# Performance work log

Measured on AMD Instinct MI355X. Metric: run time of the kernel, lower is better.

## Reference

```python
import jax, jax.numpy as jnp
import numpy as np

N = 200000   # nodes
E = 3200000  # edges
B = 1024     # graphs in batch
A = 10       # num_actions
IN, C, ED = 9, 64, 1
NEG_SLOPE = 0.2


def _xavier(k, shape):
    lim = (6.0 / (shape[0] + shape[1])) ** 0.5
    return jax.random.uniform(k, shape, jnp.float32, -lim, lim)


def setup_inputs() -> dict:
    key = jax.random.key(0)
    ks = jax.random.split(key, 24)
    x = jax.random.normal(ks[0], (N, IN), jnp.float32)
    edge_index = jax.random.randint(ks[1], (2, E), 0, N, dtype=jnp.int64)
    edge_attr = jax.random.normal(ks[2], (E, ED), jnp.float32)
    agent_state = jax.random.normal(ks[3], (B, 34), jnp.float32)
    pool_batch = jnp.sort(jax.random.randint(ks[4], (N,), 0, B, dtype=jnp.int64))
    return {
        "x": x, "edge_index": edge_index, "edge_attr": edge_attr,
        "agent_state": agent_state, "pool_batch": pool_batch,
        # GATConv params (heads=1): lin (no bias), lin_edge (no bias), att vectors, bias
        "W_gat": _xavier(ks[5], (IN, C)),
        "att_src": jax.random.normal(ks[6], (C,), jnp.float32) * 0.1,
        "att_dst": jax.random.normal(ks[7], (C,), jnp.float32) * 0.1,
        "W_edge": _xavier(ks[8], (ED, C)),
        "att_edge": jax.random.normal(ks[9], (C,), jnp.float32) * 0.1,
        "b_gat": jnp.zeros((C,), jnp.float32),
        # fc_input1: Linear(64,128)
        "W1": _xavier(ks[10], (C, 128)), "b1": jnp.zeros((128,), jnp.float32),
        # fc_input2: Linear(34,64)
        "W2": _xavier(ks[11], (34, 64)), "b2": jnp.zeros((64,), jnp.float32),
        # fc_output: Linear(192,128), Linear(128,A)
        "W3": _xavier(ks[12], (192, 128)), "b3": jnp.zeros((128,), jnp.float32),
        "W4": _xavier(ks[13], (128, A)), "b4": jnp.zeros((A,), jnp.float32),
    }


def _gat_forward(x, edge_index, edge_attr, W_gat, att_src, att_dst, W_edge, att_edge, b_gat):
    src, dst = edge_index[0], edge_index[1]
    # add self-loops; self-loop edge_attr = mean of incoming edge_attr (PyG fill_value='mean')
    ones = jnp.ones((E,), jnp.float32)
    deg = jax.ops.segment_sum(ones, dst, num_segments=N)
    loop_attr = jax.ops.segment_sum(edge_attr, dst, num_segments=N) / jnp.maximum(deg, 1.0)[:, None]
    loop_idx = jnp.arange(N, dtype=src.dtype)
    src_f = jnp.concatenate([src, loop_idx])
    dst_f = jnp.concatenate([dst, loop_idx])
    attr_f = jnp.concatenate([edge_attr, loop_attr], axis=0)  # [E+N, 1]
    h = x @ W_gat                                   # [N, C]
    a_src = h @ att_src                             # [N]
    a_dst = h @ att_dst                             # [N]
    a_edge = (attr_f @ W_edge) @ att_edge           # [E+N]
    alpha = jax.nn.leaky_relu(a_src[src_f] + a_dst[dst_f] + a_edge, NEG_SLOPE)
    # per-destination softmax (stable)
    m = jax.ops.segment_max(alpha, dst_f, num_segments=N)
    ea = jnp.exp(alpha - m[dst_f])
    denom = jax.ops.segment_sum(ea, dst_f, num_segments=N)
    coef = ea / denom[dst_f]                        # [E+N]
    out = jax.ops.segment_sum(coef[:, None] * h[src_f], dst_f, num_segments=N)
    return out + b_gat


def reference(x, edge_index, edge_attr, agent_state, pool_batch,
              W_gat, att_src, att_dst, W_edge, att_edge, b_gat,
              W1, b1, W2, b2, W3, b3, W4, b4):
    g = _gat_forward(x, edge_index, edge_attr, W_gat, att_src, att_dst, W_edge, att_edge, b_gat)
    g = jax.nn.relu(g @ W1 + b1)                    # [N, 128]
    # global mean pool per graph
    s = jax.ops.segment_sum(g, pool_batch, num_segments=B)
    cnt = jax.ops.segment_sum(jnp.ones((N,), g.dtype), pool_batch, num_segments=B)
    pooled = s / jnp.maximum(cnt, 1.0)[:, None]     # [B, 128]
    a = jax.nn.relu(agent_state @ W2 + b2)          # [B, 64]
    z = jnp.concatenate([pooled, a], axis=-1)       # [B, 192]
    z = jax.nn.relu(z @ W3 + b3)
    return z @ W4 + b4                              # [B, A]
```

## Files before the change

### kernel.cpp

```cpp
#include <hip/hip_runtime.h>
#include <hip/hip_bf16.h>

namespace {

constexpr int kN  = 200000;
constexpr int kE  = 3200000;
constexpr int kB  = 1024;
constexpr int kA  = 10;
constexpr int kIn = 9;
constexpr int kC  = 64;
constexpr int kH1 = 128;
constexpr int kAS = 34;
constexpr int kH2 = 64;
constexpr int kZ  = 192;
constexpr int kH3 = 128;
constexpr int kMAXD = 192;
constexpr int kGPB_MFMA = 10;
constexpr int kNBUCK = 782;
constexpr int kEPC  = 4096;
constexpr int kNCHK = (kE + kEPC - 1) / kEPC;
constexpr int kNODEBLK = kN / 4;

using bf16 = __hip_bfloat16;
typedef __attribute__((ext_vector_type(8))) short short8;
typedef __attribute__((ext_vector_type(4))) float f32x4;

__device__ __forceinline__ float b2f(bf16 v) { return __bfloat162float(v); }
__device__ __forceinline__ float lrelu(float x) { return x > 0.f ? x : 0.2f * x; }

__device__ __forceinline__ float ldf(const void* p, size_t i, int f32) {
  return f32 ? ((const float*)p)[i] : __bfloat162float(((const bf16*)p)[i]);
}
__device__ __forceinline__ int ldi(const void* p, size_t i, int i64) {
  return i64 ? (int)(((const long long*)p)[i]) : ((const int*)p)[i];
}

__global__ void k_init2(const void* __restrict__ ei, const void* __restrict__ x,
                        const void* __restrict__ We, const void* __restrict__ ae,
                        const void* __restrict__ Wg, const void* __restrict__ vsw,
                        const void* __restrict__ vdw, const void* __restrict__ W1,
                        const void* __restrict__ b1, const void* __restrict__ bgat,
                        int* __restrict__ flags, float* __restrict__ scal,
                        short* __restrict__ w1t, float* __restrict__ bb1) {
  __shared__ int c0, c1;
  int t = threadIdx.x;
  if (t == 0) { c0 = 0; c1 = 0; }
  __syncthreads();
  int zc = (((const int*)ei)[2 * t + 1] == 0) ? 1 : 0;
  int nc = 0;
  for (int j = t; j < 8192; j += 1024) {
    unsigned short u = ((const unsigned short*)x)[j];
    if ((u & 0x7F80u) == 0x7F80u) nc++;
  }
  atomicAdd(&c0, zc);
  atomicAdd(&c1, nc);
  __syncthreads();
  int f32 = (c1 > 3) ? 1 : 0;
  if (t == 0) { flags[0] = (c0 > 512) ? 1 : 0; flags[1] = f32; }
  int wid = t >> 6, lane = t & 63;
  if (wid == 0) {
    float p = ldf(We, lane, f32) * ldf(ae, lane, f32);
    #pragma unroll
    for (int o = 32; o > 0; o >>= 1) p += __shfl_xor(p, o);
    if (lane == 0) scal[0] = p;
  } else if (wid <= kIn) {
    int k = wid - 1;
    float w = ldf(Wg, (size_t)k * kC + lane, f32);
    float ps = w * ldf(vsw, lane, f32);
    float pd = w * ldf(vdw, lane, f32);
    #pragma unroll
    for (int o = 32; o > 0; o >>= 1) { ps += __shfl_xor(ps, o); pd += __shfl_xor(pd, o); }
    if (lane == 0) { scal[1 + k] = ps; scal[10 + k] = pd; }
  }
  for (int i = t; i < kC * kH1; i += 1024) {
    int c = i >> 6, k = i & 63;
    float v = ldf(W1, (size_t)k * kH1 + c, f32);
    w1t[i] = (short)__bfloat16_as_ushort(__float2bfloat16(v));
  }
  if (t < kH1) {
    int c = t;
    float s = ldf(b1, c, f32);
    for (int k = 0; k < kC; ++k)
      s += ldf(bgat, k, f32) * ldf(W1, (size_t)k * kH1 + c, f32);
    bb1[c] = s;
  }
}

__global__ void k_diag(const int* __restrict__ flags, float ws_mb,
                       float* __restrict__ out) {
  int i = blockIdx.x * 256 + threadIdx.x;
  if (i >= kB * kA) return;
  float v;
  if (flags) v = (1 + flags[0]) * 1e7f + (1 + flags[1]) * 1e6f + fminf(ws_mb, 999999.f);
  else       v = 3e7f + fminf(ws_mb, 999999.f);
  out[i] = v;
}

__global__ void __launch_bounds__(256) k_nodehist(
    const void* __restrict__ x, const void* __restrict__ Wg,
    const void* __restrict__ ei, const int* __restrict__ flags,
    const float* __restrict__ scal, bf16* __restrict__ hout,
    float* __restrict__ a_src, float* __restrict__ a_dst,
    int* __restrict__ blockhist) {
  int tid = threadIdx.x;
  int f32 = flags[1];
  if (blockIdx.x < kNODEBLK) {
    __shared__ float wg[kIn * kC];
    __shared__ float sc[19];
    for (int i = tid; i < kIn * kC; i += 256) wg[i] = ldf(Wg, i, f32);
    if (tid < 19) sc[tid] = scal[tid];
    __syncthreads();
    int n = blockIdx.x * 4 + (tid >> 6);
    int lane = tid & 63;
    float hc = 0.f, as_ = 0.f, ad_ = 0.f;
    #pragma unroll
    for (int k = 0; k < kIn; ++k) {
      float xv = ldf(x, (size_t)n * kIn + k, f32);
      hc  += xv * wg[k * kC + lane];
      as_ += xv * sc[1 + k];
      ad_ += xv * sc[10 + k];
    }
    hout[(size_t)n * kC + lane] = __float2bfloat16(hc);
    if (lane == 0) { a_src[n] = as_; a_dst[n] = ad_; }
  } else {
    __shared__ int hh[kNBUCK];
    int i64 = flags[0];
    int c = blockIdx.x - kNODEBLK;
    for (int i = tid; i < kNBUCK; i += 256) hh[i] = 0;
    __syncthreads();
    int e0 = c * kEPC;
    #pragma unroll
    for (int j = 0; j < 16; ++j) {
      int e = e0 + j * 256 + tid;
      if (e < kE) {
        int d = ldi(ei, (size_t)kE + e, i64);
        atomicAdd(&hh[d >> 8], 1);
      }
    }
    __syncthreads();
    for (int i = tid; i < kNBUCK; i += 256) blockhist[(size_t)i * kNCHK + c] = hh[i];
  }
}

__global__ void __launch_bounds__(256) r_scanA(int* __restrict__ blockhist,
                                               int* __restrict__ buckettot) {
  __shared__ int lds[256];
  int b = blockIdx.x, tid = threadIdx.x;
  int run = 0;
  for (int c0 = 0; c0 < kNCHK; c0 += 256) {
    int idx = c0 + tid;
    int v = (idx < kNCHK) ? blockhist[(size_t)b * kNCHK + idx] : 0;
    int xv = v;
    lds[tid] = xv;
    __syncthreads();
    #pragma unroll
    for (int o = 1; o < 256; o <<= 1) {
      int t = (tid >= o) ? lds[tid - o] : 0;
      __syncthreads();
      xv += t;
      lds[tid] = xv;
      __syncthreads();
    }
    if (idx < kNCHK) blockhist[(size_t)b * kNCHK + idx] = run + xv - v;
    run += lds[255];
    __syncthreads();
  }
  if (tid == 0) buckettot[b] = run;
}

__global__ void r_scanB(const int* __restrict__ buckettot, int* __restrict__ bucketbase) {
  __shared__ int lds[1024];
  int tid = threadIdx.x;
  int v = (tid < kNBUCK) ? buckettot[tid] : 0;
  int xv = v;
  lds[tid] = xv;
  __syncthreads();
  #pragma unroll
  for (int o = 1; o < 1024; o <<= 1) {
    int t = (tid >= o) ? lds[tid - o] : 0;
    __syncthreads();
    xv += t;
    lds[tid] = xv;
    __syncthreads();
  }
  if (tid < kNBUCK) bucketbase[tid] = xv - v;
  if (tid == kNBUCK - 1) bucketbase[kNBUCK] = xv;
}

__global__ void __launch_bounds__(256) r_scatter(
    const void* __restrict__ ei, const void* __restrict__ eattr,
    const int* __restrict__ flags, const float* __restrict__ a_src,
    const float* __restrict__ scal, const int* __restrict__ blockhist,
    const int* __restrict__ bucketbase, int2* __restrict__ mid) {
  __shared__ int cur[kNBUCK];
  int i64 = flags[0], f32 = flags[1];
  int c = blockIdx.x, tid = threadIdx.x;
  for (int i = tid; i < kNBUCK; i += 256)
    cur[i] = bucketbase[i] + blockhist[(size_t)i * kNCHK + c];
  __syncthreads();
  float sedge = scal[0];
  int e0 = c * kEPC;
  #pragma unroll
  for (int j = 0; j < 16; ++j) {
    int e = e0 + j * 256 + tid;
    if (e < kE) {
      int s = ldi(ei, e, i64);
      int d = ldi(ei, (size_t)kE + e, i64);
      float ap = a_src[s] + sedge * ldf(eattr, e, f32);
      int pos = atomicAdd(&cur[d >> 8], 1);
      mid[pos] = make_int2(s | ((d & 255) << 18), __float_as_int(ap));
    }
  }
}

__global__ void __launch_bounds__(256) r_bucket(
    const int2* __restrict__ mid, const int* __restrict__ bucketbase,
    int* __restrict__ offs, int2* __restrict__ csr) {
  __shared__ int h[256], cur[256], lds[256];
  int b = blockIdx.x, tid = threadIdx.x;
  int base = bucketbase[b];
  int cnt = bucketbase[b + 1] - base;
  h[tid] = 0;
  __syncthreads();
  for (int i = tid; i < cnt; i += 256)
    atomicAdd(&h[(mid[base + i].x >> 18) & 255], 1);
  __syncthreads();
  int v = h[tid];
  int xv = v;
  lds[tid] = xv;
  __syncthreads();
  #pragma unroll
  for (int o = 1; o < 256; o <<= 1) {
    int t = (tid >= o) ? lds[tid - o] : 0;
    __syncthreads();
    xv += t;
    lds[tid] = xv;
    __syncthreads();
  }
  int excl = xv - v;
  int n = b * 256 + tid;
  if (n < kN) offs[n] = base + excl;
  if (b == kNBUCK - 1 && tid == 0) offs[kN] = kE;
  cur[tid] = excl;
  __syncthreads();
  for (int i = tid; i < cnt; i += 256) {
    int2 e = mid[base + i];
    int dl = (e.x >> 18) & 255;
    int pos = atomicAdd(&cur[dl], 1);
    csr[base + pos] = make_int2(e.x & 0x3FFFF, e.y);
  }
}

__global__ void __launch_bounds__(256) k_gather5(
    const bf16* __restrict__ h, const float* __restrict__ a_src,
    const float* __restrict__ a_dst, const int* __restrict__ offs,
    const int2* __restrict__ csr, bf16* __restrict__ gbuf) {
  int wid = threadIdx.x >> 6, lane = threadIdx.x & 63;
  int n0 = (blockIdx.x * 4 + wid) * 4;
  for (int t = 0; t < 4; ++t) {
    int n = n0 + t;
    int base = offs[n];
    int degc = min(offs[n + 1] - base, kMAXD);
    float adst = a_dst[n], asrcn = a_src[n];
    int s0_ = 0, s1_ = 0, s2_ = 0;
    float e0_ = 0.f, e1_ = 0.f, e2_ = 0.f;
    float sap = 0.f;
    if (lane < degc) {
      int2 c = csr[base + lane];
      s0_ = c.x;
      float ap = __int_as_float(c.y);
      sap += ap - a_src[s0_];
      e0_ = __expf(fminf(lrelu(ap + adst), 60.f));
    }
    if (lane + 64 < degc) {
      int2 c = csr[base + lane + 64];
      s1_ = c.x;
      float ap = __int_as_float(c.y);
      sap += ap - a_src[s1_];
      e1_ = __expf(fminf(lrelu(ap + adst), 60.f));
    }
    if (lane + 128 < degc) {
      int2 c = csr[base + lane + 128];
      s2_ = c.x;
      float ap = __int_as_float(c.y);
      sap += ap - a_src[s2_];
      e2_ = __expf(fminf(lrelu(ap + adst), 60.f));
    }
    float se = e0_ + e1_ + e2_;
    #pragma unroll
    for (int o = 32; o > 0; o >>= 1) {
      se  += __shfl_xor(se, o);
      sap += __shfl_xor(sap, o);
    }
    float la = sap / fmaxf((float)degc, 1.0f);
    float aself = lrelu(asrcn + adst + la);
    float eself = __expf(fminf(aself, 60.f));
    float inv = 1.f / (se + eself);
    float g = eself * b2f(h[(size_t)n * kC + lane]);
    int lim = min(degc, 64);
    int j = 0;
    for (; j + 3 < lim; j += 4) {
      int sa = __shfl(s0_, j),     sb = __shfl(s0_, j + 1);
      int sc = __shfl(s0_, j + 2), sd = __shfl(s0_, j + 3);
      float ea = __shfl(e0_, j),     eb = __shfl(e0_, j + 1);
      float ec = __shfl(e0_, j + 2), ed = __shfl(e0_, j + 3);
      float ha = b2f(h[(size_t)sa * kC + lane]);
      float hb = b2f(h[(size_t)sb * kC + lane]);
      float hcv = b2f(h[(size_t)sc * kC + lane]);
      float hd = b2f(h[(size_t)sd * kC + lane]);
      g += ea * ha;
      g += eb * hb;
      g += ec * hcv;
      g += ed * hd;
    }
    for (; j < lim; ++j)
      g += __shfl(e0_, j) * b2f(h[(size_t)__shfl(s0_, j) * kC + lane]);
    if (degc > 64) {
      int lim1 = min(degc, 128) - 64;
      for (int j2 = 0; j2 < lim1; ++j2)
        g += __shfl(e1_, j2) * b2f(h[(size_t)__shfl(s1_, j2) * kC + lane]);
      if (degc > 128) {
        int lim2 = degc - 128;
        for (int j2 = 0; j2 < lim2; ++j2)
          g += __shfl(e2_, j2) * b2f(h[(size_t)__shfl(s2_, j2) * kC + lane]);
      }
    }
    gbuf[(size_t)n * kC + lane] = __float2bfloat16(g * inv);
  }
}

__global__ void __launch_bounds__(512) k_fc1mfma(
    const short* __restrict__ gbuf, const short* __restrict__ w1t,
    const float* __restrict__ bb1, const void* __restrict__ pb,
    const int* __restrict__ flags, float* __restrict__ pooled) {
  int i64 = flags[0];
  int wv = threadIdx.x >> 6, lane = threadIdx.x & 63;
  int col = lane & 15, kg = lane >> 4;
  int c = wv * 16 + col;
  short8 bf0 = *(const short8*)(w1t + (size_t)c * kC + kg * 8);
  short8 bf1 = *(const short8*)(w1t + (size_t)c * kC + 32 + kg * 8);
  float bias = bb1[c];
  int curb = -1;
  float pacc = 0.f;
  int g0 = blockIdx.x * kGPB_MFMA;
  for (int gi = 0; gi < kGPB_MFMA; ++gi) {
    int n0 = (g0 + gi) * 16;
    const short* arow = gbuf + (size_t)(n0 + col) * kC + kg * 8;
    short8 a0 = *(const short8*)(arow);
    short8 a1 = *(const short8*)(arow + 32);
    f32x4 acc = {bias, bias, bias, bias};
    acc = __builtin_amdgcn_mfma_f32_16x16x32_bf16(a0, bf0, acc, 0, 0, 0);
    acc = __builtin_amdgcn_mfma_f32_16x16x32_bf16(a1, bf1, acc, 0, 0, 0);
    #pragma unroll
    for (int r = 0; r < 4; ++r) {
      int node = n0 + kg * 4 + r;
      int b = ldi(pb, node, i64);
      float v = fmaxf(acc[r], 0.f);
      if (b != curb) {
        if (curb >= 0) atomicAdd(pooled + (size_t)curb * kH1 + c, pacc);
        curb = b;
        pacc = 0.f;
      }
      pacc += v;
    }
  }
  if (curb >= 0) atomicAdd(pooled + (size_t)curb * kH1 + c, pacc);
}

__device__ __forceinline__ int lowb(const void* pb, int i64, int target) {
  int lo = 0, hi = kN;
  while (lo < hi) {
    int mid = (lo + hi) >> 1;
    if (ldi(pb, mid, i64) < target) lo = mid + 1; else hi = mid;
  }
  return lo;
}

__global__ void k_final(const float* __restrict__ pooled, const void* __restrict__ pb,
                        const void* __restrict__ agent, const void* __restrict__ W2,
                        const void* __restrict__ b2v, const void* __restrict__ W3,
                        const void* __restrict__ b3v, const void* __restrict__ W4,
                        const void* __restrict__ b4v, const int* __restrict__ flags,
                        float* __restrict__ out) {
  __shared__ float z[kZ];
  __shared__ float t[kH3];
  int i64 = flags[0], f32 = flags[1];
  int b = blockIdx.x, l = threadIdx.x;
  int c0 = lowb(pb, i64, b);
  int c1 = lowb(pb, i64, b + 1);
  float ct = fmaxf((float)(c1 - c0), 1.0f);
  float av = ldf(b2v, l, f32);
  for (int k = 0; k < kAS; ++k)
    av += ldf(agent, (size_t)b * kAS + k, f32) * ldf(W2, (size_t)k * kH2 + l, f32);
  z[kH1 + l] = fmaxf(av, 0.f);
  z[l] = pooled[(size_t)b * kH1 + l] / ct;
  z[64 + l] = pooled[(size_t)b * kH1 + 64 + l] / ct;
  __syncthreads();
  float t0 = ldf(b3v, l, f32), t1 = ldf(b3v, 64 + l, f32);
  for (int k = 0; k < kZ; ++k) {
    float zk = z[k];
    t0 += zk * ldf(W3, (size_t)k * kH3 + l, f32);
    t1 += zk * ldf(W3, (size_t)k * kH3 + 64 + l, f32);
  }
  t[l] = fmaxf(t0, 0.f);
  t[64 + l] = fmaxf(t1, 0.f);
  __syncthreads();
  if (l < kA) {
    float o = ldf(b4v, l, f32);
    for (int k = 0; k < kH3; ++k) o += t[k] * ldf(W4, (size_t)k * kA + l, f32);
    out[b * kA + l] = o;
  }
}

}

extern "C" void kernel_launch(void* const* d_in, const int* in_sizes, int n_in,
                              void* d_out, int out_size, void* d_ws, size_t ws_size,
                              hipStream_t stream) {
  const void* x     = d_in[0];
  const void* ei    = d_in[1];
  const void* eattr = d_in[2];
  const void* agent = d_in[3];
  const void* pb    = d_in[4];
  const void* Wg    = d_in[5];
  const void* att_s = d_in[6];
  const void* att_d = d_in[7];
  const void* We    = d_in[8];
  const void* att_e = d_in[9];
  const void* bgat  = d_in[10];
  const void* W1    = d_in[11];
  const void* b1    = d_in[12];
  const void* W2    = d_in[13];
  const void* b2v   = d_in[14];
  const void* W3    = d_in[15];
  const void* b3v   = d_in[16];
  const void* W4    = d_in[17];
  const void* b4v   = d_in[18];
  float* out = (float*)d_out;

  char* ws = (char*)d_ws;
  size_t off = 0;
  auto alloc = [&](size_t bytes) -> void* {
    void* p = ws + off;
    off += (bytes + 255) & ~size_t(255);
    return p;
  };
  int*   flags  = (int*)alloc(256);
  float* pooled = (float*)alloc(size_t(kB) * kH1 * 4);
  size_t zbytes = off;
  float* scal       = (float*)alloc(256);
  short* w1t        = (short*)alloc(size_t(kC) * kH1 * 2);
  float* bb1        = (float*)alloc(size_t(kH1) * 4);
  int*   buckettot  = (int*)alloc(size_t(kNBUCK) * 4);
  int*   bucketbase = (int*)alloc((size_t(kNBUCK) + 1) * 4);
  float* a_src      = (float*)alloc(size_t(kN) * 4);
  float* a_dst      = (float*)alloc(size_t(kN) * 4);
  int*   offs       = (int*)alloc((size_t(kN) + 1) * 4);
  int*   blockhist  = (int*)alloc(size_t(kNBUCK) * kNCHK * 4);
  int2*  csr = (int2*)alloc(size_t(kE) * 8);
  bf16*  h   = (bf16*)alloc(size_t(kN) * kC * 2);
  char*  uni  = (char*)alloc(size_t(kE) * 8);
  int2*  mid  = (int2*)uni;
  bf16*  gbuf = (bf16*)uni;
  size_t need = off;

  float ws_mb = (float)(double(ws_size) / (1024.0 * 1024.0));

  if (ws_size < 4096) {
    k_diag<<<(kB * kA + 255) / 256, 256, 0, stream>>>(nullptr, ws_mb, out);
    return;
  }
  hipMemsetAsync(ws, 0, (ws_size < need) ? size_t(256) : zbytes, stream);
  k_init2<<<1, 1024, 0, stream>>>(ei, x, We, att_e, Wg, att_s, att_d, W1, b1, bgat,
                                  flags, scal, w1t, bb1);
  if (ws_size < need) {
    k_diag<<<(kB * kA + 255) / 256, 256, 0, stream>>>(flags, ws_mb, out);
    return;
  }

  k_nodehist<<<kNODEBLK + kNCHK, 256, 0, stream>>>(x, Wg, ei, flags, scal, h,
                                                   a_src, a_dst, blockhist);
  r_scanA<<<kNBUCK, 256, 0, stream>>>(blockhist, buckettot);
  r_scanB<<<1, 1024, 0, stream>>>(buckettot, bucketbase);
  r_scatter<<<kNCHK, 256, 0, stream>>>(ei, eattr, flags, a_src, scal, blockhist,
                                       bucketbase, mid);
  r_bucket<<<kNBUCK, 256, 0, stream>>>(mid, bucketbase, offs, csr);
  k_gather5<<<kN / 16, 256, 0, stream>>>(h, a_src, a_dst, offs, csr, gbuf);
  k_fc1mfma<<<kN / (16 * kGPB_MFMA), 512, 0, stream>>>((const short*)gbuf, w1t, bb1,
                                                       pb, flags, pooled);
  k_final<<<kB, 64, 0, stream>>>(pooled, pb, agent, W2, b2v, W3, b3v, W4, b4v,
                                 flags, out);
}
```

Measured before the change: 392.3 us.

## Compute FC1 and mean pool per graph block without atomics

Replaces the node-chunked FC1+pool kernel, which used atomicAdd into a zeroed pooled buffer, with one block per graph. Each block binary-searches its node range, runs the MFMA over the 16-row groups covering it, masks out-of-range rows, reduces across lanes and writes the mean directly. This removes the atomics, the per-node batch-id loads and the memset of pooled, and moves the division out of the final kernel. In exchange, boundary row groups are computed twice by neighbouring graphs, and the gbuf allocation is padded so the last group can be read past the end.

```diff
diff --git a/kernel.cpp b/kernel.cpp
--- a/kernel.cpp
+++ b/kernel.cpp
@@ -15,7 +15,6 @@
 constexpr int kZ  = 192;
 constexpr int kH3 = 128;
 constexpr int kMAXD = 192;
-constexpr int kGPB_MFMA = 10;
 constexpr int kNBUCK = 782;
 constexpr int kEPC  = 4096;
 constexpr int kNCHK = (kE + kEPC - 1) / kEPC;
@@ -329,22 +328,34 @@
   }
 }
 
-__global__ void __launch_bounds__(512) k_fc1mfma(
+__device__ __forceinline__ int lowb(const void* pb, int i64, int target) {
+  int lo = 0, hi = kN;
+  while (lo < hi) {
+    int mid = (lo + hi) >> 1;
+    if (ldi(pb, mid, i64) < target) lo = mid + 1; else hi = mid;
+  }
+  return lo;
+}
+
+__global__ void __launch_bounds__(512) k_fc1graph(
     const short* __restrict__ gbuf, const short* __restrict__ w1t,
     const float* __restrict__ bb1, const void* __restrict__ pb,
     const int* __restrict__ flags, float* __restrict__ pooled) {
   int i64 = flags[0];
+  int b = blockIdx.x;
   int wv = threadIdx.x >> 6, lane = threadIdx.x & 63;
   int col = lane & 15, kg = lane >> 4;
   int c = wv * 16 + col;
+  int c0 = lowb(pb, i64, b);
+  int c1 = lowb(pb, i64, b + 1);
+  float ct = fmaxf((float)(c1 - c0), 1.0f);
   short8 bf0 = *(const short8*)(w1t + (size_t)c * kC + kg * 8);
   short8 bf1 = *(const short8*)(w1t + (size_t)c * kC + 32 + kg * 8);
   float bias = bb1[c];
-  int curb = -1;
   float pacc = 0.f;
-  int g0 = blockIdx.x * kGPB_MFMA;
-  for (int gi = 0; gi < kGPB_MFMA; ++gi) {
-    int n0 = (g0 + gi) * 16;
+  int g0 = c0 >> 4, g1 = (c1 + 15) >> 4;
+  for (int gi = g0; gi < g1; ++gi) {
+    int n0 = gi * 16;
     const short* arow = gbuf + (size_t)(n0 + col) * kC + kg * 8;
     short8 a0 = *(const short8*)(arow);
     short8 a1 = *(const short8*)(arow + 32);
@@ -354,29 +365,16 @@
     #pragma unroll
     for (int r = 0; r < 4; ++r) {
       int node = n0 + kg * 4 + r;
-      int b = ldi(pb, node, i64);
       float v = fmaxf(acc[r], 0.f);
-      if (b != curb) {
-        if (curb >= 0) atomicAdd(pooled + (size_t)curb * kH1 + c, pacc);
-        curb = b;
-        pacc = 0.f;
-      }
-      pacc += v;
-    }
-  }
-  if (curb >= 0) atomicAdd(pooled + (size_t)curb * kH1 + c, pacc);
-}
-
-__device__ __forceinline__ int lowb(const void* pb, int i64, int target) {
-  int lo = 0, hi = kN;
-  while (lo < hi) {
-    int mid = (lo + hi) >> 1;
-    if (ldi(pb, mid, i64) < target) lo = mid + 1; else hi = mid;
-  }
-  return lo;
-}
-
-__global__ void k_final(const float* __restrict__ pooled, const void* __restrict__ pb,
+      pacc += (node >= c0 && node < c1) ? v : 0.f;
+    }
+  }
+  pacc += __shfl_xor(pacc, 16);
+  pacc += __shfl_xor(pacc, 32);
+  if (kg == 0) pooled[(size_t)b * kH1 + c] = pacc / ct;
+}
+
+__global__ void k_final(const float* __restrict__ pooled,
                         const void* __restrict__ agent, const void* __restrict__ W2,
                         const void* __restrict__ b2v, const void* __restrict__ W3,
                         const void* __restrict__ b3v, const void* __restrict__ W4,
@@ -384,17 +382,14 @@
                         float* __restrict__ out) {
   __shared__ float z[kZ];
   __shared__ float t[kH3];
-  int i64 = flags[0], f32 = flags[1];
+  int f32 = flags[1];
   int b = blockIdx.x, l = threadIdx.x;
-  int c0 = lowb(pb, i64, b);
-  int c1 = lowb(pb, i64, b + 1);
-  float ct = fmaxf((float)(c1 - c0), 1.0f);
   float av = ldf(b2v, l, f32);
   for (int k = 0; k < kAS; ++k)
     av += ldf(agent, (size_t)b * kAS + k, f32) * ldf(W2, (size_t)k * kH2 + l, f32);
   z[kH1 + l] = fmaxf(av, 0.f);
-  z[l] = pooled[(size_t)b * kH1 + l] / ct;
-  z[64 + l] = pooled[(size_t)b * kH1 + 64 + l] / ct;
+  z[l] = pooled[(size_t)b * kH1 + l];
+  z[64 + l] = pooled[(size_t)b * kH1 + 64 + l];
   __syncthreads();
   float t0 = ldf(b3v, l, f32), t1 = ldf(b3v, 64 + l, f32);
   for (int k = 0; k < kZ; ++k) {
@@ -446,8 +441,8 @@
     return p;
   };
   int*   flags  = (int*)alloc(256);
-  float* pooled = (float*)alloc(size_t(kB) * kH1 * 4);
   size_t zbytes = off;
+  float* pooled     = (float*)alloc(size_t(kB) * kH1 * 4);
   float* scal       = (float*)alloc(256);
   short* w1t        = (short*)alloc(size_t(kC) * kH1 * 2);
   float* bb1        = (float*)alloc(size_t(kH1) * 4);
@@ -459,7 +454,7 @@
   int*   blockhist  = (int*)alloc(size_t(kNBUCK) * kNCHK * 4);
   int2*  csr = (int2*)alloc(size_t(kE) * 8);
   bf16*  h   = (bf16*)alloc(size_t(kN) * kC * 2);
-  char*  uni  = (char*)alloc(size_t(kE) * 8);
+  char*  uni  = (char*)alloc(size_t(kE) * 8 + 4096);
   int2*  mid  = (int2*)uni;
   bf16*  gbuf = (bf16*)uni;
   size_t need = off;
@@ -486,8 +481,7 @@
                                        bucketbase, mid);
   r_bucket<<<kNBUCK, 256, 0, stream>>>(mid, bucketbase, offs, csr);
   k_gather5<<<kN / 16, 256, 0, stream>>>(h, a_src, a_dst, offs, csr, gbuf);
-  k_fc1mfma<<<kN / (16 * kGPB_MFMA), 512, 0, stream>>>((const short*)gbuf, w1t, bb1,
-                                                       pb, flags, pooled);
-  k_final<<<kB, 64, 0, stream>>>(pooled, pb, agent, W2, b2v, W3, b3v, W4, b4v,
+  k_fc1graph<<<kB, 512, 0, stream>>>((const short*)gbuf, w1t, bb1, pb, flags, pooled);
+  k_final<<<kB, 64, 0, stream>>>(pooled, agent, W2, b2v, W3, b3v, W4, b4v,
                                  flags, out);
 }
```

After: 374.8 us. 1.05x faster.
